# Kernel optimization log

Measured on AMD Instinct MI355X. Metric: run time of the kernel, lower is better.

Reference implementation:

```python
import jax, jax.numpy as jnp
import numpy as np

WS = 8        # window_size
SHIFT = 4     # shift_size
NH = 6        # num_heads
EPS = 1e-5


def _rel_pos_index(ws):
    coords = np.stack(np.meshgrid(np.arange(ws), np.arange(ws), indexing='ij'))  # [2,ws,ws]
    cf = coords.reshape(2, -1)                      # [2, ws*ws]
    rel = cf[:, :, None] - cf[:, None, :]           # [2, N, N]
    rel = rel.transpose(1, 2, 0)                    # [N, N, 2]
    rel[:, :, 0] += ws - 1
    rel[:, :, 1] += ws - 1
    rel[:, :, 0] *= 2 * ws - 1
    return rel.sum(-1)                              # [N, N] int


def _attn_mask(H, W, ws, shift):
    img = np.zeros((H, W), dtype=np.float32)
    slices = (slice(0, -ws), slice(-ws, -shift), slice(-shift, None))
    cnt = 0
    for hs in slices:
        for wsl in slices:
            img[hs, wsl] = cnt
            cnt += 1
    mw = img.reshape(H // ws, ws, W // ws, ws).transpose(0, 2, 1, 3).reshape(-1, ws * ws)
    diff = mw[:, None, :] - mw[:, :, None]          # [nW, N, N]
    return np.where(diff != 0, -100.0, 0.0).astype(np.float32)


def _layernorm(x, g, b):
    mu = x.mean(-1, keepdims=True)
    var = ((x - mu) ** 2).mean(-1, keepdims=True)
    return (x - mu) * jax.lax.rsqrt(var + EPS) * g + b


def setup_inputs() -> dict:
    key = jax.random.key(0)
    ks = jax.random.split(key, 8)
    C, HID = 192, 768
    return {
        'x': jax.random.normal(ks[0], (8, 128, 128, C), jnp.float32),
        'g1': jnp.ones((C,), jnp.float32),
        'b1': jnp.zeros((C,), jnp.float32),
        'qkv_w': jax.random.normal(ks[1], (3 * C, C), jnp.float32) * 0.02,
        'qkv_b': jnp.zeros((3 * C,), jnp.float32),
        'rpb_table': jax.random.normal(ks[2], ((2 * WS - 1) ** 2, NH), jnp.float32) * 0.02,
        'proj_w': jax.random.normal(ks[3], (C, C), jnp.float32) * 0.02,
        'proj_b': jnp.zeros((C,), jnp.float32),
        'g2': jnp.ones((C,), jnp.float32),
        'b2': jnp.zeros((C,), jnp.float32),
        'fc1_w': jax.random.normal(ks[4], (HID, C), jnp.float32) * 0.02,
        'fc1_b': jnp.zeros((HID,), jnp.float32),
        'fc2_w': jax.random.normal(ks[5], (C, HID), jnp.float32) * 0.02,
        'fc2_b': jnp.zeros((C,), jnp.float32),
    }


def reference(x, g1, b1, qkv_w, qkv_b, rpb_table, proj_w, proj_b, g2, b2,
              fc1_w, fc1_b, fc2_w, fc2_b):
    B, H, W, C = x.shape
    N = WS * WS
    hd = C // NH
    scale = hd ** -0.5

    rpi = jnp.asarray(_rel_pos_index(WS))                 # [N,N] static
    mask = jnp.asarray(_attn_mask(H, W, WS, SHIFT))       # [nW,N,N] static
    nW = mask.shape[0]

    shortcut = x.reshape(B, H * W, C)
    xn = _layernorm(shortcut, g1, b1).reshape(B, H, W, C)

    # cyclic shift
    xs = jnp.roll(xn, shift=(-SHIFT, -SHIFT), axis=(1, 2))

    # window partition -> [B*nW, N, C]
    win = xs.reshape(B, H // WS, WS, W // WS, WS, C).transpose(0, 1, 3, 2, 4, 5)
    win = win.reshape(-1, N, C)
    B_ = win.shape[0]

    # qkv
    qkv = jnp.einsum('bnc,oc->bno', win, qkv_w) + qkv_b   # [B_,N,3C]
    qkv = qkv.reshape(B_, N, 3, NH, hd).transpose(2, 0, 3, 1, 4)  # [3,B_,NH,N,hd]
    q, k, v = qkv[0] * scale, qkv[1], qkv[2]

    attn = jnp.einsum('bhnd,bhmd->bhnm', q, k)            # [B_,NH,N,N]
    bias = rpb_table[rpi.reshape(-1)].reshape(N, N, NH).transpose(2, 0, 1)
    attn = attn + bias[None]
    attn = attn.reshape(B, nW, NH, N, N) + mask[None, :, None]
    attn = jax.nn.softmax(attn.reshape(B_, NH, N, N), axis=-1)

    out = jnp.einsum('bhnm,bhmd->bhnd', attn, v)          # [B_,NH,N,hd]
    out = out.transpose(0, 2, 1, 3).reshape(B_, N, C)
    out = jnp.einsum('bnc,oc->bno', out, proj_w) + proj_b

    # window reverse -> [B,H,W,C]
    out = out.reshape(B, H // WS, W // WS, WS, WS, C).transpose(0, 1, 3, 2, 4, 5)
    out = out.reshape(B, H, W, C)
    out = jnp.roll(out, shift=(SHIFT, SHIFT), axis=(1, 2)).reshape(B, H * W, C)

    x1 = shortcut + out
    h = _layernorm(x1, g2, b2)
    h = jnp.einsum('bnc,hc->bnh', h, fc1_w) + fc1_b
    h = jax.nn.gelu(h, approximate=False)
    h = jnp.einsum('bnh,ch->bnc', h, fc2_w) + fc2_b
    x2 = x1 + h
    return x2.reshape(B, H, W, C)
```

## Files before the change

kernel.cpp:

```cpp
#include <hip/hip_runtime.h>
#include <hip/hip_bf16.h>

typedef __attribute__((ext_vector_type(8))) short s16x8;
typedef __attribute__((ext_vector_type(4))) float f32x4;

__device__ __forceinline__ unsigned short f2bf(float f){
    __hip_bfloat16 h = __float2bfloat16(f);
    return *reinterpret_cast<unsigned short*>(&h);
}

__device__ __forceinline__ int flab(int g){ return (g < 120) ? 0 : ((g < 124) ? 1 : 2); }

__device__ __forceinline__ void async16(const void* g, void* l){
    __builtin_amdgcn_global_load_lds(
        (const __attribute__((address_space(1))) unsigned int*)g,
        (__attribute__((address_space(3))) unsigned int*)l, 16, 0, 0);
}

__global__ __launch_bounds__(256) void wconv_all(
    const float* __restrict__ w0, const float* __restrict__ w1,
    const float* __restrict__ w2, const float* __restrict__ w3,
    unsigned short* __restrict__ o0, unsigned short* __restrict__ o1,
    unsigned short* __restrict__ o2, unsigned short* __restrict__ o3)
{
    int i = blockIdx.x*256 + threadIdx.x;
    if (i < 110592) o0[i] = f2bf(w0[i]);
    if (i < 36864)  o1[i] = f2bf(w1[i]);
    if (i < 147456) {
        int o = i/192, k = i - o*192;
        int oc = o/96, r = o - oc*96, ks = k>>5, c = k&31;
        o2[((oc*6 + ks)*96 + r)*32 + c] = f2bf(w2[i]);
    }
    if (i < 147456) {
        int o = i/768, k = i - o*768;
        int q = o/48, r = o - q*48, ks = k>>5, c = k&31;
        o3[((q*24 + ks)*48 + r)*32 + c] = f2bf(w3[i]);
    }
}

__global__ __launch_bounds__(256) void lnqkv_kernel(
    const float* __restrict__ x, const float* __restrict__ g1, const float* __restrict__ b1,
    const unsigned short* __restrict__ wq, const float* __restrict__ qkvb,
    unsigned short* __restrict__ qo, unsigned short* __restrict__ ko,
    unsigned short* __restrict__ vo)
{
    __shared__ __attribute__((aligned(16))) unsigned short win[64*200];
    __shared__ __attribute__((aligned(16))) unsigned short Bs[64*200];
    const int b_ = blockIdx.x;
    const int bb = b_>>8, wi = b_&255, wh = wi>>4, ww = wi&15;
    const int tid = threadIdx.x;
    const int wv = tid>>6, lane = tid&63, lrow = lane&15, quad = lane>>4;

    {
        const int n = tid>>2, q4 = tid&3;
        const int r = n>>3, c = n&7;
        const int hh = (wh*8 + r + 4)&127, wp = (ww*8 + c + 4)&127;
        const float* px = x + (((size_t)bb*128+hh)*128+wp)*192 + q4*48;
        float v[48];
        #pragma unroll
        for (int m=0;m<12;++m) *(float4*)(v+m*4) = *(const float4*)(px+m*4);
        float s = 0.f;
        #pragma unroll
        for (int k=0;k<48;++k) s += v[k];
        s += __shfl_xor(s,1); s += __shfl_xor(s,2);
        float mu = s*(1.0f/192.0f);
        float qv = 0.f;
        #pragma unroll
        for (int k=0;k<48;++k){ float d=v[k]-mu; qv += d*d; }
        qv += __shfl_xor(qv,1); qv += __shfl_xor(qv,2);
        float rstd = rsqrtf(qv*(1.0f/192.0f) + 1e-5f);
        const float* pg = g1 + q4*48;
        const float* pb = b1 + q4*48;
        unsigned short* pw = win + n*200 + q4*48;
        #pragma unroll
        for (int k=0;k<48;++k) pw[k] = f2bf((v[k]-mu)*rstd*pg[k] + pb[k]);
    }
    __syncthreads();

    s16x8 af[6];
    #pragma unroll
    for (int kc=0;kc<6;++kc)
        af[kc] = *(const s16x8*)(win + (wv*16+lrow)*200 + kc*32 + quad*8);

    for (int ot=0; ot<9; ++ot) {
        const int o0 = ot*64;
        __syncthreads();
        #pragma unroll
        for (int t=0;t<6;++t) {
            int cid = tid + t*256;
            *(int4*)(Bs + (cid/24)*200 + (cid%24)*8) =
                *(const int4*)(wq + (size_t)o0*192 + cid*8);
        }
        __syncthreads();
        f32x4 acc[4];
        #pragma unroll
        for (int j=0;j<4;++j) acc[j] = (f32x4){0.f,0.f,0.f,0.f};
        #pragma unroll
        for (int kc=0;kc<6;++kc)
            #pragma unroll
            for (int j=0;j<4;++j) {
                s16x8 bf = *(const s16x8*)(Bs + (j*16+lrow)*200 + kc*32 + quad*8);
                acc[j] = __builtin_amdgcn_mfma_f32_16x16x32_bf16(af[kc], bf, acc[j], 0, 0, 0);
            }
        __syncthreads();
        unsigned short* T = Bs;
        const int part = ot/3;
        float bv[4];
        #pragma unroll
        for (int j=0;j<4;++j) bv[j] = qkvb[o0 + j*16 + lrow];

        if (part < 2) {
            const float scale = (part==0) ? 0.17677669529663687f : 1.0f;
            #pragma unroll
            for (int j=0;j<4;++j)
                #pragma unroll
                for (int rg=0;rg<4;++rg) {
                    int n2 = wv*16 + quad*4 + rg;
                    T[n2*72 + j*16 + lrow] = f2bf((acc[j][rg]+bv[j])*scale);
                }
            __syncthreads();
            unsigned short* dst = (part==0) ? qo : ko;
            #pragma unroll
            for (int t=0;t<2;++t) {
                int c = tid + t*256;
                int n2 = c>>3, blk = c&7;
                int o_in = o0 + blk*8 - part*192;
                int head = o_in>>5, d = o_in&31;
                *(int4*)(dst + (((size_t)b_*6+head)*64 + n2)*32 + d) =
                    *(const int4*)(T + n2*72 + blk*8);
            }
        } else {
            #pragma unroll
            for (int j=0;j<4;++j)
                #pragma unroll
                for (int rg=0;rg<4;++rg) {
                    int n2 = wv*16 + quad*4 + rg;
                    T[(j*16+lrow)*72 + n2] = f2bf(acc[j][rg]+bv[j]);
                }
            __syncthreads();
            #pragma unroll
            for (int t=0;t<2;++t) {
                int c = tid + t*256;
                int ol = c>>3, nb = (c&7)*8;
                int o_in = o0 + ol - 384;
                int head = o_in>>5, d = o_in&31;
                *(int4*)(vo + (((size_t)b_*6+head)*32 + d)*64 + nb) =
                    *(const int4*)(T + ol*72 + nb);
            }
        }
    }
}

__global__ __launch_bounds__(384) void attn_kernel(
    const unsigned short* __restrict__ q, const unsigned short* __restrict__ k,
    const unsigned short* __restrict__ vT, const float* __restrict__ rpb,
    unsigned short* __restrict__ ao)
{
    __shared__ float rpb_s[1350];
    __shared__ __attribute__((aligned(16))) unsigned short p_lds[6*4608];
    const int b_ = blockIdx.x;
    const int h = threadIdx.x >> 6;
    const int lane = threadIdx.x & 63, lrow = lane & 15, quad = lane >> 4;
    for (int i = threadIdx.x; i < 1350; i += 384) rpb_s[i] = rpb[i];
    __syncthreads();

    const size_t hb = ((size_t)b_*6 + h)*2048;
    const unsigned short* qb = q  + hb;
    const unsigned short* kb = k  + hb;
    const unsigned short* vb = vT + hb;

    s16x8 qf[4], kf[4];
    #pragma unroll
    for (int i = 0; i < 4; ++i) qf[i] = *(const s16x8*)(qb + (i*16+lrow)*32 + quad*8);
    #pragma unroll
    for (int j = 0; j < 4; ++j) kf[j] = *(const s16x8*)(kb + (j*16+lrow)*32 + quad*8);

    const f32x4 zz = {0.f,0.f,0.f,0.f};
    f32x4 s[4][4];
    #pragma unroll
    for (int i = 0; i < 4; ++i)
        #pragma unroll
        for (int j = 0; j < 4; ++j)
            s[i][j] = __builtin_amdgcn_mfma_f32_16x16x32_bf16(qf[i], kf[j], zz, 0, 0, 0);

    const int wi = b_ & 255, wh = wi >> 4, ww = wi & 15;
    int labm[4];
    #pragma unroll
    for (int j = 0; j < 4; ++j) {
        int m = j*16 + lrow;
        labm[j] = flab(wh*8 + (m >> 3))*3 + flab(ww*8 + (m & 7));
    }
    unsigned short* pl = p_lds + h*4608;
    #pragma unroll
    for (int i = 0; i < 4; ++i) {
        #pragma unroll
        for (int rg = 0; rg < 4; ++rg) {
            int n = i*16 + quad*4 + rg;
            int rn = n >> 3, cn = n & 7;
            int labn = flab(wh*8 + rn)*3 + flab(ww*8 + cn);
            float vals[4];
            float vmax = -1e30f;
            #pragma unroll
            for (int j = 0; j < 4; ++j) {
                int m = j*16 + lrow;
                int idx = ((rn - (m >> 3) + 7)*15 + (cn - (m & 7) + 7))*6 + h;
                float val = s[i][j][rg] + rpb_s[idx];
                if (labn != labm[j]) val -= 100.f;
                vals[j] = val;
                vmax = fmaxf(vmax, val);
            }
            #pragma unroll
            for (int o = 1; o < 16; o <<= 1) vmax = fmaxf(vmax, __shfl_xor(vmax, o));
            float sum = 0.f;
            #pragma unroll
            for (int j = 0; j < 4; ++j) { vals[j] = __expf(vals[j] - vmax); sum += vals[j]; }
            #pragma unroll
            for (int o = 1; o < 16; o <<= 1) sum += __shfl_xor(sum, o);
            float inv = 1.f / sum;
            #pragma unroll
            for (int j = 0; j < 4; ++j) pl[n*72 + j*16 + lrow] = f2bf(vals[j]*inv);
        }
    }
    __syncthreads();

    f32x4 oacc[4][2];
    #pragma unroll
    for (int i = 0; i < 4; ++i) { oacc[i][0] = zz; oacc[i][1] = zz; }
    #pragma unroll
    for (int kc = 0; kc < 2; ++kc) {
        s16x8 vf[2];
        #pragma unroll
        for (int jd = 0; jd < 2; ++jd)
            vf[jd] = *(const s16x8*)(vb + (jd*16+lrow)*64 + kc*32 + quad*8);
        #pragma unroll
        for (int i = 0; i < 4; ++i) {
            s16x8 pf = *(const s16x8*)(pl + (i*16+lrow)*72 + kc*32 + quad*8);
            #pragma unroll
            for (int jd = 0; jd < 2; ++jd)
                oacc[i][jd] = __builtin_amdgcn_mfma_f32_16x16x32_bf16(pf, vf[jd], oacc[i][jd], 0, 0, 0);
        }
    }
    unsigned short* ob = ao + (size_t)b_*12288 + h*32;
    #pragma unroll
    for (int i = 0; i < 4; ++i)
        #pragma unroll
        for (int jd = 0; jd < 2; ++jd)
            #pragma unroll
            for (int rg = 0; rg < 4; ++rg) {
                int n = i*16 + quad*4 + rg;
                ob[(size_t)n*192 + jd*16 + lrow] = f2bf(oacc[i][jd][rg]);
            }
}

__device__ __forceinline__ void mm64x192(
    const unsigned short* __restrict__ A, const unsigned short* __restrict__ W,
    size_t m0, unsigned short* As, unsigned short* Bs, f32x4 (&acc)[12])
{
    const int tid = threadIdx.x, wv = tid>>6, lane = tid&63;
    const int lrow = lane&15, quad = lane>>4;
    const int grow = lane>>2;
    const int gcb  = (lane&3) ^ ((lane>>3)&3);
    #pragma unroll
    for (int j=0;j<12;++j) acc[j] = (f32x4){0.f,0.f,0.f,0.f};

    const unsigned short* Ab = A + (m0 + grow)*192 + gcb*8;
    const unsigned short* Wb = W + (size_t)grow*192 + gcb*8;

    auto issue = [&](int k0, unsigned short* Ad, unsigned short* Bd) {
        async16(Ab + (size_t)(wv*16)*192 + k0,     Ad + wv*512);
        async16(Wb + (size_t)(wv*16)*192 + k0,     Bd + wv*512);
        async16(Wb + (size_t)((wv+4)*16)*192 + k0, Bd + (wv+4)*512);
        async16(Wb + (size_t)((wv+8)*16)*192 + k0, Bd + (wv+8)*512);
    };
    issue(0, As, Bs);
    int cur = 0;
    for (int k0=0; k0<192; k0+=32) {
        __syncthreads();
        if (k0+32 < 192) issue(k0+32, As + (cur^1)*2048, Bs + (cur^1)*6144);
        const unsigned short* Ac = As + cur*2048;
        const unsigned short* Bc = Bs + cur*6144;
        const int rs = (quad ^ ((lrow>>1)&3)) << 3;
        s16x8 af = *(const s16x8*)(Ac + (wv*16+lrow)*32 + rs);
        #pragma unroll
        for (int j=0;j<12;++j) {
            s16x8 bf = *(const s16x8*)(Bc + (j*16+lrow)*32 + rs);
            acc[j] = __builtin_amdgcn_mfma_f32_16x16x32_bf16(af, bf, acc[j], 0, 0, 0);
        }
        cur ^= 1;
    }
}

__global__ __launch_bounds__(256) void projln_kernel(
    const unsigned short* __restrict__ A, const unsigned short* __restrict__ W,
    const float* __restrict__ pbias, const float* __restrict__ x,
    const float* __restrict__ g2, const float* __restrict__ b2,
    float* __restrict__ x1, unsigned short* __restrict__ xln2b)
{
    __shared__ __attribute__((aligned(16))) char smem[32768];
    unsigned short* As = (unsigned short*)smem;
    unsigned short* Bs = (unsigned short*)(smem + 8192);
    const int b_ = blockIdx.x;
    const int tid = threadIdx.x, wv = tid>>6, lane = tid&63;
    const int lrow = lane&15, quad = lane>>4;
    const size_t m0 = (size_t)b_*64;

    f32x4 acc[12];
    mm64x192(A, W, m0, As, Bs, acc);
    __syncthreads();

    const int bb = b_>>8, wi = b_&255, wh = wi>>4, ww = wi&15;
    float bv[12], gv[12], b2v[12];
    #pragma unroll
    for (int j=0;j<12;++j) {
        bv[j]  = pbias[j*16+lrow];
        gv[j]  = g2[j*16+lrow];
        b2v[j] = b2[j*16+lrow];
    }
    unsigned short* T = (unsigned short*)smem;
    #pragma unroll
    for (int rg=0;rg<4;++rg) {
        int n2 = wv*16 + quad*4 + rg;
        int r = n2>>3, c = n2&7;
        int hh = (wh*8+r+4)&127, wp = (ww*8+c+4)&127;
        size_t tok = ((size_t)bb*128+hh)*128 + wp;
        float xv[12];
        float s = 0.f;
        #pragma unroll
        for (int j=0;j<12;++j) {
            float t = acc[j][rg] + bv[j] + x[tok*192 + j*16 + lrow];
            xv[j] = t; s += t;
        }
        #pragma unroll
        for (int o=1;o<16;o<<=1) s += __shfl_xor(s, o);
        float mu = s*(1.0f/192.0f);
        float qv = 0.f;
        #pragma unroll
        for (int j=0;j<12;++j){ float d = xv[j]-mu; qv += d*d; }
        #pragma unroll
        for (int o=1;o<16;o<<=1) qv += __shfl_xor(qv, o);
        float rstd = rsqrtf(qv*(1.0f/192.0f) + 1e-5f);
        #pragma unroll
        for (int j=0;j<12;++j) {
            x1[tok*192 + j*16 + lrow] = xv[j];
            T[n2*200 + j*16 + lrow] = f2bf((xv[j]-mu)*rstd*gv[j] + b2v[j]);
        }
    }
    __syncthreads();
    #pragma unroll
    for (int t=0;t<6;++t) {
        int cid = tid + t*256;
        int n2 = cid/24, blk = cid%24;
        int r = n2>>3, c = n2&7;
        int hh = (wh*8+r+4)&127, wp = (ww*8+c+4)&127;
        size_t tok = ((size_t)bb*128+hh)*128 + wp;
        int row = (int)(tok & 127);
        int ks = blk>>2, kb = blk&3;
        int sw = (kb ^ ((row>>1)&3)) << 3;
        *(int4*)(xln2b + (tok>>7)*24576 + ks*4096 + row*32 + sw) =
            *(const int4*)(T + n2*200 + blk*8);
    }
}

__global__ __launch_bounds__(512, 2) void mlp_kernel(
    const unsigned short* __restrict__ Ablk,
    const unsigned short* __restrict__ W1b,
    const float* __restrict__ fc1b,
    const unsigned short* __restrict__ W2b,
    const float* __restrict__ fc2b,
    const float* __restrict__ x1, float* __restrict__ out)
{
    __shared__ __attribute__((aligned(16))) unsigned short Ald[6*2048];
    __shared__ __attribute__((aligned(16))) unsigned short Hld[24*2048];
    const int b_ = blockIdx.x;
    const int mt = b_>>1, half = b_&1;
    const int tid = threadIdx.x, wv = tid>>6, lane = tid&63;
    const int lrow = lane&15, quad = lane>>4;
    const int rs = (quad ^ ((lrow>>1)&3)) << 3;

    {
        const unsigned short* src = Ablk + (size_t)mt*24576 + half*2048 + lane*8;
        #pragma unroll
        for (int r=0;r<3;++r) {
            int c = r*8 + wv;
            async16(src + (c>>2)*4096 + (c&3)*512, Ald + c*512);
        }
    }
    __syncthreads();

    f32x4 acc[4][6];
    #pragma unroll
    for (int i=0;i<4;++i)
        #pragma unroll
        for (int j=0;j<6;++j) acc[i][j] = (f32x4){0.f,0.f,0.f,0.f};
    #pragma unroll 2
    for (int ks=0;ks<6;++ks) {
        s16x8 af[4], bf[6];
        #pragma unroll
        for (int i=0;i<4;++i)
            af[i] = *(const s16x8*)(Ald + ks*2048 + (i*16+lrow)*32 + rs);
        #pragma unroll
        for (int j=0;j<6;++j)
            bf[j] = *(const s16x8*)(W1b + (size_t)((wv*6+ks)*96 + j*16+lrow)*32 + quad*8);
        #pragma unroll
        for (int i=0;i<4;++i)
            #pragma unroll
            for (int j=0;j<6;++j)
                acc[i][j] = __builtin_amdgcn_mfma_f32_16x16x32_bf16(af[i], bf[j], acc[i][j], 0, 0, 0);
    }

    {
        float bv1[6];
        #pragma unroll
        for (int j=0;j<6;++j) bv1[j] = fc1b[wv*96 + j*16 + lrow];
        #pragma unroll
        for (int i=0;i<4;++i)
            #pragma unroll
            for (int j=0;j<6;++j)
                #pragma unroll
                for (int rg=0;rg<4;++rg) {
                    int row = i*16 + quad*4 + rg;
                    int o = wv*96 + j*16 + lrow;
                    float v = acc[i][j][rg] + bv1[j];
                    float v2 = v*v;
                    float z = v*(1.5957691216057308f + 0.07135481627f*v2);
                    float r = v * __builtin_amdgcn_rcpf(1.f + __expf(-z));
                    int ksh = o>>5, c5 = o&31;
                    Hld[ksh*2048 + row*32 + (((c5>>3) ^ ((row>>1)&3))<<3) + (c5&7)] = f2bf(r);
                }
    }
    __syncthreads();

    const int r0 = (wv>>2)*32, c0 = (wv&3)*48;
    f32x4 a2[2][3];
    #pragma unroll
    for (int i=0;i<2;++i)
        #pragma unroll
        for (int j=0;j<3;++j) a2[i][j] = (f32x4){0.f,0.f,0.f,0.f};
    #pragma unroll 4
    for (int ks=0;ks<24;++ks) {
        s16x8 af2[2], bf2[3];
        #pragma unroll
        for (int i=0;i<2;++i)
            af2[i] = *(const s16x8*)(Hld + ks*2048 + (r0 + i*16 + lrow)*32 + rs);
        #pragma unroll
        for (int j=0;j<3;++j)
            bf2[j] = *(const s16x8*)(W2b + (size_t)(((wv&3)*24 + ks)*48 + j*16+lrow)*32 + quad*8);
        #pragma unroll
        for (int i=0;i<2;++i)
            #pragma unroll
            for (int j=0;j<3;++j)
                a2[i][j] = __builtin_amdgcn_mfma_f32_16x16x32_bf16(af2[i], bf2[j], a2[i][j], 0, 0, 0);
    }

    {
        float bv2[3];
        #pragma unroll
        for (int j=0;j<3;++j) bv2[j] = fc2b[c0 + j*16 + lrow];
        #pragma unroll
        for (int i=0;i<2;++i)
            #pragma unroll
            for (int j=0;j<3;++j)
                #pragma unroll
                for (int rg=0;rg<4;++rg) {
                    size_t grow = (size_t)mt*128 + half*64 + r0 + i*16 + quad*4 + rg;
                    size_t ad = grow*192 + c0 + j*16 + lrow;
                    out[ad] = a2[i][j][rg] + bv2[j] + x1[ad];
                }
    }
}

extern "C" void kernel_launch(void* const* d_in, const int* in_sizes, int n_in,
                              void* d_out, int out_size, void* d_ws, size_t ws_size,
                              hipStream_t stream)
{
    const float* x      = (const float*)d_in[0];
    const float* g1     = (const float*)d_in[1];
    const float* b1     = (const float*)d_in[2];
    const float* qkv_w  = (const float*)d_in[3];
    const float* qkv_b  = (const float*)d_in[4];
    const float* rpb    = (const float*)d_in[5];
    const float* proj_w = (const float*)d_in[6];
    const float* proj_b = (const float*)d_in[7];
    const float* g2     = (const float*)d_in[8];
    const float* b2     = (const float*)d_in[9];
    const float* fc1_w  = (const float*)d_in[10];
    const float* fc1_b  = (const float*)d_in[11];
    const float* fc2_w  = (const float*)d_in[12];
    const float* fc2_b  = (const float*)d_in[13];
    float* out = (float*)d_out;
    char* ws = (char*)d_ws;

    if (ws_size < 353206272ULL) return;

    unsigned short* qbuf  = (unsigned short*)(ws + 0);
    unsigned short* kbuf  = (unsigned short*)(ws + 50331648);
    unsigned short* vbuf  = (unsigned short*)(ws + 100663296);
    unsigned short* attnO = (unsigned short*)(ws + 150994944);
    float*          x1    = (float*)        (ws + 201326592);
    unsigned short* xln2  = (unsigned short*)(ws + 301989888);
    unsigned short* wq    = (unsigned short*)(ws + 352321536);
    unsigned short* wp    = (unsigned short*)(ws + 352321536 + 221184);
    unsigned short* w1b   = (unsigned short*)(ws + 352321536 + 221184 + 73728);
    unsigned short* w2b   = (unsigned short*)(ws + 352321536 + 221184 + 73728 + 294912);

    wconv_all<<<576, 256, 0, stream>>>(qkv_w, proj_w, fc1_w, fc2_w, wq, wp, w1b, w2b);
    lnqkv_kernel<<<2048, 256, 0, stream>>>(x, g1, b1, wq, qkv_b, qbuf, kbuf, vbuf);
    attn_kernel<<<2048, 384, 0, stream>>>(qbuf, kbuf, vbuf, rpb, attnO);
    projln_kernel<<<2048, 256, 0, stream>>>(attnO, wp, proj_b, x, g2, b2, x1, xln2);
    mlp_kernel<<<2048, 512, 0, stream>>>(xln2, w1b, fc1_b, w2b, fc2_b, x1, out);
}
```

Baseline: 581.7 us.

## Chunk MLP hidden dimension into four slices to shrink LDS and raise occupancy

```diff
diff --git a/kernel.cpp b/kernel.cpp
--- a/kernel.cpp
+++ b/kernel.cpp
@@ -28,8 +28,8 @@
     if (i < 36864)  o1[i] = f2bf(w1[i]);
     if (i < 147456) {
         int o = i/192, k = i - o*192;
-        int oc = o/96, r = o - oc*96, ks = k>>5, c = k&31;
-        o2[((oc*6 + ks)*96 + r)*32 + c] = f2bf(w2[i]);
+        int oc = o/192, r = o - oc*192, ks = k>>5, c = k&31;
+        o2[((oc*6 + ks)*192 + r)*32 + c] = f2bf(w2[i]);
     }
     if (i < 147456) {
         int o = i/768, k = i - o*768;
@@ -361,7 +361,7 @@
     }
 }
 
-__global__ __launch_bounds__(512, 2) void mlp_kernel(
+__global__ __launch_bounds__(512, 4) void mlp_kernel(
     const unsigned short* __restrict__ Ablk,
     const unsigned short* __restrict__ W1b,
     const float* __restrict__ fc1b,
@@ -370,11 +370,13 @@
     const float* __restrict__ x1, float* __restrict__ out)
 {
     __shared__ __attribute__((aligned(16))) unsigned short Ald[6*2048];
-    __shared__ __attribute__((aligned(16))) unsigned short Hld[24*2048];
+    __shared__ __attribute__((aligned(16))) unsigned short Hld[6*2048];
     const int b_ = blockIdx.x;
     const int mt = b_>>1, half = b_&1;
     const int tid = threadIdx.x, wv = tid>>6, lane = tid&63;
     const int lrow = lane&15, quad = lane>>4;
+    const int wr = wv>>2, wc = wv&3;
+    const int r0 = wr*32, c0 = wc*48;
     const int rs = (quad ^ ((lrow>>1)&3)) << 3;
 
     {
@@ -385,71 +387,79 @@
             async16(src + (c>>2)*4096 + (c&3)*512, Ald + c*512);
         }
     }
+
+    float bv1[4][3];
+    #pragma unroll
+    for (int oc=0;oc<4;++oc)
+        #pragma unroll
+        for (int j=0;j<3;++j) bv1[oc][j] = fc1b[oc*192 + c0 + j*16 + lrow];
+
+    f32x4 a2[2][3];
+    #pragma unroll
+    for (int i=0;i<2;++i)
+        #pragma unroll
+        for (int j=0;j<3;++j) a2[i][j] = (f32x4){0.f,0.f,0.f,0.f};
+
     __syncthreads();
 
-    f32x4 acc[4][6];
-    #pragma unroll
-    for (int i=0;i<4;++i)
-        #pragma unroll
-        for (int j=0;j<6;++j) acc[i][j] = (f32x4){0.f,0.f,0.f,0.f};
-    #pragma unroll 2
-    for (int ks=0;ks<6;++ks) {
-        s16x8 af[4], bf[6];
-        #pragma unroll
-        for (int i=0;i<4;++i)
-            af[i] = *(const s16x8*)(Ald + ks*2048 + (i*16+lrow)*32 + rs);
-        #pragma unroll
-        for (int j=0;j<6;++j)
-            bf[j] = *(const s16x8*)(W1b + (size_t)((wv*6+ks)*96 + j*16+lrow)*32 + quad*8);
-        #pragma unroll
-        for (int i=0;i<4;++i)
-            #pragma unroll
-            for (int j=0;j<6;++j)
-                acc[i][j] = __builtin_amdgcn_mfma_f32_16x16x32_bf16(af[i], bf[j], acc[i][j], 0, 0, 0);
-    }
-
-    {
-        float bv1[6];
-        #pragma unroll
-        for (int j=0;j<6;++j) bv1[j] = fc1b[wv*96 + j*16 + lrow];
-        #pragma unroll
-        for (int i=0;i<4;++i)
-            #pragma unroll
-            for (int j=0;j<6;++j)
+    for (int oc=0; oc<4; ++oc) {
+        f32x4 a1[2][3];
+        #pragma unroll
+        for (int i=0;i<2;++i)
+            #pragma unroll
+            for (int j=0;j<3;++j) a1[i][j] = (f32x4){0.f,0.f,0.f,0.f};
+        const unsigned short* w1p = W1b + (size_t)(oc*6)*6144 + (size_t)(c0)*32 + quad*8;
+        #pragma unroll
+        for (int ks=0;ks<6;++ks) {
+            s16x8 af[2], bf[3];
+            #pragma unroll
+            for (int i=0;i<2;++i)
+                af[i] = *(const s16x8*)(Ald + ks*2048 + (r0 + i*16 + lrow)*32 + rs);
+            #pragma unroll
+            for (int j=0;j<3;++j)
+                bf[j] = *(const s16x8*)(w1p + (size_t)ks*6144 + (j*16 + lrow)*32);
+            #pragma unroll
+            for (int i=0;i<2;++i)
+                #pragma unroll
+                for (int j=0;j<3;++j)
+                    a1[i][j] = __builtin_amdgcn_mfma_f32_16x16x32_bf16(af[i], bf[j], a1[i][j], 0, 0, 0);
+        }
+
+        if (oc) __syncthreads();
+
+        #pragma unroll
+        for (int i=0;i<2;++i)
+            #pragma unroll
+            for (int j=0;j<3;++j)
                 #pragma unroll
                 for (int rg=0;rg<4;++rg) {
-                    int row = i*16 + quad*4 + rg;
-                    int o = wv*96 + j*16 + lrow;
-                    float v = acc[i][j][rg] + bv1[j];
+                    int row = r0 + i*16 + quad*4 + rg;
+                    int o = c0 + j*16 + lrow;
+                    float v = a1[i][j][rg] + bv1[oc][j];
                     float v2 = v*v;
                     float z = v*(1.5957691216057308f + 0.07135481627f*v2);
                     float r = v * __builtin_amdgcn_rcpf(1.f + __expf(-z));
                     int ksh = o>>5, c5 = o&31;
                     Hld[ksh*2048 + row*32 + (((c5>>3) ^ ((row>>1)&3))<<3) + (c5&7)] = f2bf(r);
                 }
-    }
-    __syncthreads();
-
-    const int r0 = (wv>>2)*32, c0 = (wv&3)*48;
-    f32x4 a2[2][3];
-    #pragma unroll
-    for (int i=0;i<2;++i)
-        #pragma unroll
-        for (int j=0;j<3;++j) a2[i][j] = (f32x4){0.f,0.f,0.f,0.f};
-    #pragma unroll 4
-    for (int ks=0;ks<24;++ks) {
-        s16x8 af2[2], bf2[3];
-        #pragma unroll
-        for (int i=0;i<2;++i)
-            af2[i] = *(const s16x8*)(Hld + ks*2048 + (r0 + i*16 + lrow)*32 + rs);
-        #pragma unroll
-        for (int j=0;j<3;++j)
-            bf2[j] = *(const s16x8*)(W2b + (size_t)(((wv&3)*24 + ks)*48 + j*16+lrow)*32 + quad*8);
-        #pragma unroll
-        for (int i=0;i<2;++i)
+        __syncthreads();
+
+        const unsigned short* w2p = W2b + (size_t)(wc*24 + oc*6)*1536 + quad*8;
+        #pragma unroll
+        for (int ksl=0;ksl<6;++ksl) {
+            s16x8 af2[2], bf2[3];
+            #pragma unroll
+            for (int i=0;i<2;++i)
+                af2[i] = *(const s16x8*)(Hld + ksl*2048 + (r0 + i*16 + lrow)*32 + rs);
             #pragma unroll
             for (int j=0;j<3;++j)
-                a2[i][j] = __builtin_amdgcn_mfma_f32_16x16x32_bf16(af2[i], bf2[j], a2[i][j], 0, 0, 0);
+                bf2[j] = *(const s16x8*)(w2p + (size_t)ksl*1536 + (j*16 + lrow)*32);
+            #pragma unroll
+            for (int i=0;i<2;++i)
+                #pragma unroll
+                for (int j=0;j<3;++j)
+                    a2[i][j] = __builtin_amdgcn_mfma_f32_16x16x32_bf16(af2[i], bf2[j], a2[i][j], 0, 0, 0);
+        }
     }
 
     {
```

New measurement: 556.2 us. -4.4%, faster.
